# Optimization experiments

Measured on AMD Instinct MI355X. Metric: run time of the kernel, lower is better.

Reference implementation:

```python
import jax, jax.numpy as jnp
import numpy as np

B, N = 512, 500  # batch (cells), n_nodes (genes)


def setup_inputs() -> dict:
    key = jax.random.key(0)
    k1, k2, k3, k4 = jax.random.split(key, 4)
    x = jax.random.normal(k1, (B, N), dtype=jnp.float32)
    # GumbelAdjacency edge logits (bicycle initializes these near a constant; random here)
    log_alpha = jax.random.normal(k2, (N, N), dtype=jnp.float32)
    # single Linear(n_nodes, n_nodes, bias=False) weight, torch layout [out, in]
    W = jax.random.normal(k3, (N, N), dtype=jnp.float32) / np.sqrt(N).astype(np.float32)
    # uniform noise consumed by the gumbel-sigmoid sampler (one draw per batch element)
    u = jax.random.uniform(k4, (B, N, N), dtype=jnp.float32)
    return {"x": x, "log_alpha": log_alpha, "W": W, "u": u}


def reference(x, log_alpha, W, u):
    # --- GumbelAdjacency.forward(num_batch): hard gumbel-sigmoid sample, tau=1 ---
    eps = 1e-6
    uc = jnp.clip(u, eps, 1.0 - eps)
    logistic = jnp.log(uc) - jnp.log(1.0 - uc)            # logistic(0,1) noise
    y_soft = jax.nn.sigmoid(log_alpha[None, :, :] + logistic)  # [B, N, N]
    y_hard = (y_soft > 0.5).astype(y_soft.dtype)
    adj = y_soft + jax.lax.stop_gradient(y_hard - y_soft)  # straight-through

    # --- per-node masked MLP loop, fused ---
    # original: f_x[b, i] = tanh( (mask_i * adj[b, :, i] * x[b]) @ W.T )[i]
    #                     = tanh( sum_{j != i} W[i, j] * adj[b, j, i] * x[b, j] )
    mask = 1.0 - jnp.eye(N, dtype=x.dtype)                # mask[j, i] = 0 iff j == i
    gated = adj * mask[None, :, :]                        # [B, j, i]
    f_x = jnp.tanh(jnp.einsum('bji,bj,ij->bi', gated, x, W))  # [B, N]
    return f_x
```

## Files before the change

### kernel.cpp

```cpp
#include <hip/hip_runtime.h>
#include <math.h>

#define NN 500
#define BB 512
#define BGRP 4
#define NCHUNK 10
#define JCH (NN / NCHUNK)
#define NPAIR (NN / 2)

using f2 = __attribute__((ext_vector_type(2))) float;

__device__ __forceinline__ bool np_decision(float laf, float v) {
    float l1 = (float)log((double)v);
    float s  = 1.0f - v;
    float l2 = (float)log((double)s);
    float logistic = l1 - l2;
    float z  = laf + logistic;
    float e  = (float)exp(-(double)z);
    float d  = 1.0f + e;
    float y  = 1.0f / d;
    return y > 0.5f;
}

__global__ void prep_kernel(const float* __restrict__ la,
                            const float* __restrict__ W,
                            float2* __restrict__ WU) {
    int idx = blockIdx.x * blockDim.x + threadIdx.x;
    if (idx >= NN * NN) return;
    int j = idx / NN;
    int i = idx - j * NN;
    float laf = la[idx];

    const float LO = 1e-6f;
    const float HI = (float)(1.0 - 1e-6);

    float U;
    if (!np_decision(laf, HI)) {
        U = __builtin_inff();
    } else if (np_decision(laf, LO)) {
        U = 0.0f;
    } else {
        unsigned lo = __float_as_uint(LO);
        unsigned hi = __float_as_uint(HI);
        double T  = 1.0 / (1.0 + exp((double)laf));
        float  Tf = fminf(fmaxf((float)T, LO), HI);
        unsigned g = __float_as_uint(Tf);
        unsigned a = (g > lo + 32u) ? g - 32u : lo;
        unsigned b = (g + 32u < hi) ? g + 32u : hi;
        if (a > lo) {
            if (np_decision(laf, __uint_as_float(a))) hi = a; else lo = a;
        }
        if (b > lo && b < hi) {
            if (np_decision(laf, __uint_as_float(b))) hi = b; else lo = b;
        }
        while (hi - lo > 1u) {
            unsigned mid = lo + (hi - lo) / 2u;
            if (np_decision(laf, __uint_as_float(mid))) hi = mid; else lo = mid;
        }
        U = __uint_as_float(hi);
    }
    float w = (i == j) ? 0.0f : W[i * NN + j];
    WU[idx] = make_float2(w, U);
}

__global__ __launch_bounds__(256) void fused_kernel(
        const float* __restrict__ x,
        const float* __restrict__ u,
        const float4* __restrict__ WU4,
        float* __restrict__ P) {
    __shared__ float xs[BGRP][JCH];
    const int bid = blockIdx.x;
    const int bg = bid / NCHUNK;
    const int c  = bid - bg * NCHUNK;
    const int b0 = bg * BGRP;
    const int j0 = c * JCH;
    const int t = threadIdx.x;
    if (t < BGRP * JCH) {
        int bl = t / JCH;
        int j  = t - bl * JCH;
        xs[bl][j] = x[(b0 + bl) * NN + j0 + j];
    }
    __syncthreads();
    if (t >= NPAIR) return;

    const f2* __restrict__ u0 = (const f2*)(u + (size_t)(b0 + 0) * NN * NN);
    const f2* __restrict__ u1 = (const f2*)(u + (size_t)(b0 + 1) * NN * NN);
    const f2* __restrict__ u2 = (const f2*)(u + (size_t)(b0 + 2) * NN * NN);
    const f2* __restrict__ u3 = (const f2*)(u + (size_t)(b0 + 3) * NN * NN);

    float a00 = 0.0f, a01 = 0.0f, a10 = 0.0f, a11 = 0.0f;
    float a20 = 0.0f, a21 = 0.0f, a30 = 0.0f, a31 = 0.0f;
    int k = j0 * NPAIR + t;
#pragma unroll 5
    for (int j = 0; j < JCH; ++j, k += NPAIR) {
        float4 wv = WU4[k];
        f2 v0 = __builtin_nontemporal_load(u0 + k);
        f2 v1 = __builtin_nontemporal_load(u1 + k);
        f2 v2 = __builtin_nontemporal_load(u2 + k);
        f2 v3 = __builtin_nontemporal_load(u3 + k);
        float x0 = xs[0][j], x1 = xs[1][j], x2 = xs[2][j], x3 = xs[3][j];
        if (v0.x >= wv.y) a00 += wv.x * x0;
        if (v0.y >= wv.w) a01 += wv.z * x0;
        if (v1.x >= wv.y) a10 += wv.x * x1;
        if (v1.y >= wv.w) a11 += wv.z * x1;
        if (v2.x >= wv.y) a20 += wv.x * x2;
        if (v2.y >= wv.w) a21 += wv.z * x2;
        if (v3.x >= wv.y) a30 += wv.x * x3;
        if (v3.y >= wv.w) a31 += wv.z * x3;
    }
    float* Pb = P + ((size_t)c * BB + b0) * NN;
    ((float2*)(Pb + 0 * NN))[t] = make_float2(a00, a01);
    ((float2*)(Pb + 1 * NN))[t] = make_float2(a10, a11);
    ((float2*)(Pb + 2 * NN))[t] = make_float2(a20, a21);
    ((float2*)(Pb + 3 * NN))[t] = make_float2(a30, a31);
}

__global__ __launch_bounds__(256) void reduce_kernel(const float* __restrict__ P,
                                                     float* __restrict__ out) {
    int n4 = blockIdx.x * blockDim.x + threadIdx.x;
    if (n4 >= BB * NN / 4) return;
    const int S = BB * NN;
    float4 s = ((const float4*)P)[n4];
#pragma unroll
    for (int cc = 1; cc < NCHUNK; ++cc) {
        float4 p = ((const float4*)(P + (size_t)cc * S))[n4];
        s.x += p.x; s.y += p.y; s.z += p.z; s.w += p.w;
    }
    ((float4*)out)[n4] = make_float4(tanhf(s.x), tanhf(s.y), tanhf(s.z), tanhf(s.w));
}

extern "C" void kernel_launch(void* const* d_in, const int* in_sizes, int n_in,
                              void* d_out, int out_size, void* d_ws, size_t ws_size,
                              hipStream_t stream) {
    const float* x  = (const float*)d_in[0];
    const float* la = (const float*)d_in[1];
    const float* W  = (const float*)d_in[2];
    const float* u  = (const float*)d_in[3];
    float* out = (float*)d_out;

    float2* WU = (float2*)d_ws;
    float*  P  = (float*)((char*)d_ws + (size_t)NN * NN * sizeof(float2));

    int prep_blocks = (NN * NN + 255) / 256;
    prep_kernel<<<prep_blocks, 256, 0, stream>>>(la, W, WU);
    fused_kernel<<<(BB / BGRP) * NCHUNK, 256, 0, stream>>>(x, u, (const float4*)WU, P);
    reduce_kernel<<<(BB * NN / 4 + 255) / 256, 256, 0, stream>>>(P, out);
}
```

Measured before the change: 669.1 us.

## Fuse chunk reduction into main kernel via last-block atomic counter

Measured after the change: 1.010 ms. 1.51x slower.

```diff
diff --git a/kernel.cpp b/kernel.cpp
--- a/kernel.cpp
+++ b/kernel.cpp
@@ -4,6 +4,7 @@
 #define NN 500
 #define BB 512
 #define BGRP 4
+#define BBG (BB / BGRP)
 #define NCHUNK 10
 #define JCH (NN / NCHUNK)
 #define NPAIR (NN / 2)
@@ -24,8 +25,10 @@
 
 __global__ void prep_kernel(const float* __restrict__ la,
                             const float* __restrict__ W,
-                            float2* __restrict__ WU) {
+                            float2* __restrict__ WU,
+                            int* __restrict__ cnt) {
     int idx = blockIdx.x * blockDim.x + threadIdx.x;
+    if (idx < BBG) cnt[idx] = 0;
     if (idx >= NN * NN) return;
     int j = idx / NN;
     int i = idx - j * NN;
@@ -45,8 +48,8 @@
         double T  = 1.0 / (1.0 + exp((double)laf));
         float  Tf = fminf(fmaxf((float)T, LO), HI);
         unsigned g = __float_as_uint(Tf);
-        unsigned a = (g > lo + 32u) ? g - 32u : lo;
-        unsigned b = (g + 32u < hi) ? g + 32u : hi;
+        unsigned a = (g > lo + 8u) ? g - 8u : lo;
+        unsigned b = (g + 8u < hi) ? g + 8u : hi;
         if (a > lo) {
             if (np_decision(laf, __uint_as_float(a))) hi = a; else lo = a;
         }
@@ -67,8 +70,11 @@
         const float* __restrict__ x,
         const float* __restrict__ u,
         const float4* __restrict__ WU4,
-        float* __restrict__ P) {
+        float* __restrict__ P,
+        int* __restrict__ cnt,
+        float* __restrict__ out) {
     __shared__ float xs[BGRP][JCH];
+    __shared__ int sh_last;
     const int bid = blockIdx.x;
     const int bg = bid / NCHUNK;
     const int c  = bid - bg * NCHUNK;
@@ -81,52 +87,61 @@
         xs[bl][j] = x[(b0 + bl) * NN + j0 + j];
     }
     __syncthreads();
-    if (t >= NPAIR) return;
 
-    const f2* __restrict__ u0 = (const f2*)(u + (size_t)(b0 + 0) * NN * NN);
-    const f2* __restrict__ u1 = (const f2*)(u + (size_t)(b0 + 1) * NN * NN);
-    const f2* __restrict__ u2 = (const f2*)(u + (size_t)(b0 + 2) * NN * NN);
-    const f2* __restrict__ u3 = (const f2*)(u + (size_t)(b0 + 3) * NN * NN);
+    if (t < NPAIR) {
+        const f2* __restrict__ u0 = (const f2*)(u + (size_t)(b0 + 0) * NN * NN);
+        const f2* __restrict__ u1 = (const f2*)(u + (size_t)(b0 + 1) * NN * NN);
+        const f2* __restrict__ u2 = (const f2*)(u + (size_t)(b0 + 2) * NN * NN);
+        const f2* __restrict__ u3 = (const f2*)(u + (size_t)(b0 + 3) * NN * NN);
 
-    float a00 = 0.0f, a01 = 0.0f, a10 = 0.0f, a11 = 0.0f;
-    float a20 = 0.0f, a21 = 0.0f, a30 = 0.0f, a31 = 0.0f;
-    int k = j0 * NPAIR + t;
+        float a00 = 0.0f, a01 = 0.0f, a10 = 0.0f, a11 = 0.0f;
+        float a20 = 0.0f, a21 = 0.0f, a30 = 0.0f, a31 = 0.0f;
+        int k = j0 * NPAIR + t;
 #pragma unroll 5
-    for (int j = 0; j < JCH; ++j, k += NPAIR) {
-        float4 wv = WU4[k];
-        f2 v0 = __builtin_nontemporal_load(u0 + k);
-        f2 v1 = __builtin_nontemporal_load(u1 + k);
-        f2 v2 = __builtin_nontemporal_load(u2 + k);
-        f2 v3 = __builtin_nontemporal_load(u3 + k);
-        float x0 = xs[0][j], x1 = xs[1][j], x2 = xs[2][j], x3 = xs[3][j];
-        if (v0.x >= wv.y) a00 += wv.x * x0;
-        if (v0.y >= wv.w) a01 += wv.z * x0;
-        if (v1.x >= wv.y) a10 += wv.x * x1;
-        if (v1.y >= wv.w) a11 += wv.z * x1;
-        if (v2.x >= wv.y) a20 += wv.x * x2;
-        if (v2.y >= wv.w) a21 += wv.z * x2;
-        if (v3.x >= wv.y) a30 += wv.x * x3;
-        if (v3.y >= wv.w) a31 += wv.z * x3;
+        for (int j = 0; j < JCH; ++j, k += NPAIR) {
+            float4 wv = WU4[k];
+            f2 v0 = __builtin_nontemporal_load(u0 + k);
+            f2 v1 = __builtin_nontemporal_load(u1 + k);
+            f2 v2 = __builtin_nontemporal_load(u2 + k);
+            f2 v3 = __builtin_nontemporal_load(u3 + k);
+            float x0 = xs[0][j], x1 = xs[1][j], x2 = xs[2][j], x3 = xs[3][j];
+            if (v0.x >= wv.y) a00 += wv.x * x0;
+            if (v0.y >= wv.w) a01 += wv.z * x0;
+            if (v1.x >= wv.y) a10 += wv.x * x1;
+            if (v1.y >= wv.w) a11 += wv.z * x1;
+            if (v2.x >= wv.y) a20 += wv.x * x2;
+            if (v2.y >= wv.w) a21 += wv.z * x2;
+            if (v3.x >= wv.y) a30 += wv.x * x3;
+            if (v3.y >= wv.w) a31 += wv.z * x3;
+        }
+        float* Pb = P + ((size_t)c * BB + b0) * NN;
+        ((float2*)(Pb + 0 * NN))[t] = make_float2(a00, a01);
+        ((float2*)(Pb + 1 * NN))[t] = make_float2(a10, a11);
+        ((float2*)(Pb + 2 * NN))[t] = make_float2(a20, a21);
+        ((float2*)(Pb + 3 * NN))[t] = make_float2(a30, a31);
     }
-    float* Pb = P + ((size_t)c * BB + b0) * NN;
-    ((float2*)(Pb + 0 * NN))[t] = make_float2(a00, a01);
-    ((float2*)(Pb + 1 * NN))[t] = make_float2(a10, a11);
-    ((float2*)(Pb + 2 * NN))[t] = make_float2(a20, a21);
-    ((float2*)(Pb + 3 * NN))[t] = make_float2(a30, a31);
-}
 
-__global__ __launch_bounds__(256) void reduce_kernel(const float* __restrict__ P,
-                                                     float* __restrict__ out) {
-    int n4 = blockIdx.x * blockDim.x + threadIdx.x;
-    if (n4 >= BB * NN / 4) return;
-    const int S = BB * NN;
-    float4 s = ((const float4*)P)[n4];
+    __threadfence();
+    __syncthreads();
+    if (t == 0) {
+        int old = __hip_atomic_fetch_add(&cnt[bg], 1, __ATOMIC_ACQ_REL,
+                                         __HIP_MEMORY_SCOPE_AGENT);
+        sh_last = (old == NCHUNK - 1);
+    }
+    __syncthreads();
+    if (!sh_last) return;
+    __threadfence();
+
+    for (int o = t; o < BGRP * NN; o += 256) {
+        int bl = o / NN;
+        int i  = o - bl * NN;
+        const float* Pp = P + (size_t)(b0 + bl) * NN + i;
+        float s = Pp[0];
 #pragma unroll
-    for (int cc = 1; cc < NCHUNK; ++cc) {
-        float4 p = ((const float4*)(P + (size_t)cc * S))[n4];
-        s.x += p.x; s.y += p.y; s.z += p.z; s.w += p.w;
+        for (int cc = 1; cc < NCHUNK; ++cc)
+            s += Pp[(size_t)cc * BB * NN];
+        out[(b0 + bl) * NN + i] = tanhf(s);
     }
-    ((float4*)out)[n4] = make_float4(tanhf(s.x), tanhf(s.y), tanhf(s.z), tanhf(s.w));
 }
 
 extern "C" void kernel_launch(void* const* d_in, const int* in_sizes, int n_in,
@@ -140,9 +155,10 @@
 
     float2* WU = (float2*)d_ws;
     float*  P  = (float*)((char*)d_ws + (size_t)NN * NN * sizeof(float2));
+    int*    cnt = (int*)((char*)d_ws + (size_t)NN * NN * sizeof(float2)
+                                     + (size_t)NCHUNK * BB * NN * sizeof(float));
 
     int prep_blocks = (NN * NN + 255) / 256;
-    prep_kernel<<<prep_blocks, 256, 0, stream>>>(la, W, WU);
-    fused_kernel<<<(BB / BGRP) * NCHUNK, 256, 0, stream>>>(x, u, (const float4*)WU, P);
-    reduce_kernel<<<(BB * NN / 4 + 255) / 256, 256, 0, stream>>>(P, out);
+    prep_kernel<<<prep_blocks, 256, 0, stream>>>(la, W, WU, cnt);
+    fused_kernel<<<BBG * NCHUNK, 256, 0, stream>>>(x, u, (const float4*)WU, P, cnt, out);
 }
```

## Widen fused kernel to float4 loads with software-prefetched loop and finer chunks

Applied to the files above, without the earlier changes.

Result: slower. 686.0 us (+2.5%).

```diff
diff --git a/kernel.cpp b/kernel.cpp
--- a/kernel.cpp
+++ b/kernel.cpp
@@ -4,11 +4,10 @@
 #define NN 500
 #define BB 512
 #define BGRP 4
-#define NCHUNK 10
+#define BBG (BB / BGRP)
+#define NCHUNK 20
 #define JCH (NN / NCHUNK)
-#define NPAIR (NN / 2)
-
-using f2 = __attribute__((ext_vector_type(2))) float;
+#define NQ (NN / 4)
 
 __device__ __forceinline__ bool np_decision(float laf, float v) {
     float l1 = (float)log((double)v);
@@ -45,8 +44,8 @@
         double T  = 1.0 / (1.0 + exp((double)laf));
         float  Tf = fminf(fmaxf((float)T, LO), HI);
         unsigned g = __float_as_uint(Tf);
-        unsigned a = (g > lo + 32u) ? g - 32u : lo;
-        unsigned b = (g + 32u < hi) ? g + 32u : hi;
+        unsigned a = (g > lo + 8u) ? g - 8u : lo;
+        unsigned b = (g + 8u < hi) ? g + 8u : hi;
         if (a > lo) {
             if (np_decision(laf, __uint_as_float(a))) hi = a; else lo = a;
         }
@@ -63,7 +62,29 @@
     WU[idx] = make_float2(w, U);
 }
 
-__global__ __launch_bounds__(256) void fused_kernel(
+#define CONSUME(A0_, A1_, A2_, A3_, Wa_, Wb_, jj_)                          \
+    do {                                                                     \
+        float x0 = xs[0][jj_], x1 = xs[1][jj_];                              \
+        float x2 = xs[2][jj_], x3 = xs[3][jj_];                              \
+        a00 += (A0_.x >= Wa_.y) ? Wa_.x * x0 : 0.0f;                         \
+        a01 += (A0_.y >= Wa_.w) ? Wa_.z * x0 : 0.0f;                         \
+        a02 += (A0_.z >= Wb_.y) ? Wb_.x * x0 : 0.0f;                         \
+        a03 += (A0_.w >= Wb_.w) ? Wb_.z * x0 : 0.0f;                         \
+        a10 += (A1_.x >= Wa_.y) ? Wa_.x * x1 : 0.0f;                         \
+        a11 += (A1_.y >= Wa_.w) ? Wa_.z * x1 : 0.0f;                         \
+        a12 += (A1_.z >= Wb_.y) ? Wb_.x * x1 : 0.0f;                         \
+        a13 += (A1_.w >= Wb_.w) ? Wb_.z * x1 : 0.0f;                         \
+        a20 += (A2_.x >= Wa_.y) ? Wa_.x * x2 : 0.0f;                         \
+        a21 += (A2_.y >= Wa_.w) ? Wa_.z * x2 : 0.0f;                         \
+        a22 += (A2_.z >= Wb_.y) ? Wb_.x * x2 : 0.0f;                         \
+        a23 += (A2_.w >= Wb_.w) ? Wb_.z * x2 : 0.0f;                         \
+        a30 += (A3_.x >= Wa_.y) ? Wa_.x * x3 : 0.0f;                         \
+        a31 += (A3_.y >= Wa_.w) ? Wa_.z * x3 : 0.0f;                         \
+        a32 += (A3_.z >= Wb_.y) ? Wb_.x * x3 : 0.0f;                         \
+        a33 += (A3_.w >= Wb_.w) ? Wb_.z * x3 : 0.0f;                         \
+    } while (0)
+
+__global__ __launch_bounds__(128) void fused_kernel(
         const float* __restrict__ x,
         const float* __restrict__ u,
         const float4* __restrict__ WU4,
@@ -81,38 +102,40 @@
         xs[bl][j] = x[(b0 + bl) * NN + j0 + j];
     }
     __syncthreads();
-    if (t >= NPAIR) return;
+    if (t >= NQ) return;
 
-    const f2* __restrict__ u0 = (const f2*)(u + (size_t)(b0 + 0) * NN * NN);
-    const f2* __restrict__ u1 = (const f2*)(u + (size_t)(b0 + 1) * NN * NN);
-    const f2* __restrict__ u2 = (const f2*)(u + (size_t)(b0 + 2) * NN * NN);
-    const f2* __restrict__ u3 = (const f2*)(u + (size_t)(b0 + 3) * NN * NN);
+    const float4* __restrict__ u0 = (const float4*)(u + (size_t)(b0 + 0) * NN * NN);
+    const float4* __restrict__ u1 = (const float4*)(u + (size_t)(b0 + 1) * NN * NN);
+    const float4* __restrict__ u2 = (const float4*)(u + (size_t)(b0 + 2) * NN * NN);
+    const float4* __restrict__ u3 = (const float4*)(u + (size_t)(b0 + 3) * NN * NN);
 
-    float a00 = 0.0f, a01 = 0.0f, a10 = 0.0f, a11 = 0.0f;
-    float a20 = 0.0f, a21 = 0.0f, a30 = 0.0f, a31 = 0.0f;
-    int k = j0 * NPAIR + t;
-#pragma unroll 5
-    for (int j = 0; j < JCH; ++j, k += NPAIR) {
-        float4 wv = WU4[k];
-        f2 v0 = __builtin_nontemporal_load(u0 + k);
-        f2 v1 = __builtin_nontemporal_load(u1 + k);
-        f2 v2 = __builtin_nontemporal_load(u2 + k);
-        f2 v3 = __builtin_nontemporal_load(u3 + k);
-        float x0 = xs[0][j], x1 = xs[1][j], x2 = xs[2][j], x3 = xs[3][j];
-        if (v0.x >= wv.y) a00 += wv.x * x0;
-        if (v0.y >= wv.w) a01 += wv.z * x0;
-        if (v1.x >= wv.y) a10 += wv.x * x1;
-        if (v1.y >= wv.w) a11 += wv.z * x1;
-        if (v2.x >= wv.y) a20 += wv.x * x2;
-        if (v2.y >= wv.w) a21 += wv.z * x2;
-        if (v3.x >= wv.y) a30 += wv.x * x3;
-        if (v3.y >= wv.w) a31 += wv.z * x3;
+    float a00 = 0.0f, a01 = 0.0f, a02 = 0.0f, a03 = 0.0f;
+    float a10 = 0.0f, a11 = 0.0f, a12 = 0.0f, a13 = 0.0f;
+    float a20 = 0.0f, a21 = 0.0f, a22 = 0.0f, a23 = 0.0f;
+    float a30 = 0.0f, a31 = 0.0f, a32 = 0.0f, a33 = 0.0f;
+
+    int k  = j0 * NQ + t;
+    int kw = j0 * (2 * NQ) + 2 * t;
+
+    float4 A0 = u0[k], A1 = u1[k], A2 = u2[k], A3 = u3[k];
+    float4 Wa = WU4[kw], Wb = WU4[kw + 1];
+
+#pragma unroll 4
+    for (int j = 0; j < JCH - 1; ++j) {
+        const int k2 = k + NQ, kw2 = kw + 2 * NQ;
+        float4 B0 = u0[k2], B1 = u1[k2], B2 = u2[k2], B3 = u3[k2];
+        float4 Wc = WU4[kw2], Wd = WU4[kw2 + 1];
+        CONSUME(A0, A1, A2, A3, Wa, Wb, j);
+        A0 = B0; A1 = B1; A2 = B2; A3 = B3; Wa = Wc; Wb = Wd;
+        k = k2; kw = kw2;
     }
+    CONSUME(A0, A1, A2, A3, Wa, Wb, JCH - 1);
+
     float* Pb = P + ((size_t)c * BB + b0) * NN;
-    ((float2*)(Pb + 0 * NN))[t] = make_float2(a00, a01);
-    ((float2*)(Pb + 1 * NN))[t] = make_float2(a10, a11);
-    ((float2*)(Pb + 2 * NN))[t] = make_float2(a20, a21);
-    ((float2*)(Pb + 3 * NN))[t] = make_float2(a30, a31);
+    ((float4*)(Pb + 0 * NN))[t] = make_float4(a00, a01, a02, a03);
+    ((float4*)(Pb + 1 * NN))[t] = make_float4(a10, a11, a12, a13);
+    ((float4*)(Pb + 2 * NN))[t] = make_float4(a20, a21, a22, a23);
+    ((float4*)(Pb + 3 * NN))[t] = make_float4(a30, a31, a32, a33);
 }
 
 __global__ __launch_bounds__(256) void reduce_kernel(const float* __restrict__ P,
@@ -143,6 +166,6 @@
 
     int prep_blocks = (NN * NN + 255) / 256;
     prep_kernel<<<prep_blocks, 256, 0, stream>>>(la, W, WU);
-    fused_kernel<<<(BB / BGRP) * NCHUNK, 256, 0, stream>>>(x, u, (const float4*)WU, P);
+    fused_kernel<<<BBG * NCHUNK, 128, 0, stream>>>(x, u, (const float4*)WU, P);
     reduce_kernel<<<(BB * NN / 4 + 255) / 256, 256, 0, stream>>>(P, out);
 }
```
